# Kernel tuning notes

Hardware: AMD Instinct MI355X
Metric: run time of the kernel (lower is better)

The kernel has to match this reference:

```python
import jax, jax.numpy as jnp
import numpy as np

PATCH = 288
DIM = 2048
SCALE = DIM ** -0.5
NUM_INSTANCE = 4
B, Q, H, W = 32, 16, 24, 12


def _layernorm(x):
    # elementwise_affine=False LayerNorm, eps=1e-5
    m = jnp.mean(x, axis=-1, keepdims=True)
    v = jnp.mean((x - m) ** 2, axis=-1, keepdims=True)
    return (x - m) / jnp.sqrt(v + 1e-5)


def _l2norm(x):
    n = jnp.sqrt(jnp.sum(x * x, axis=-1, keepdims=True))
    return x / jnp.maximum(n, 1e-12)


def _catcher(x, g, cam_embed, Wq, Wg, pos_embed):
    # x: [B,Q,C] queries; g: [B,N,C] tokens; cam_embed: [B*N//PATCH,1,C] or None
    rel_q = jnp.einsum('bqc,dc->bqd', x, Wq)
    Bg, N, C = g.shape
    G = Bg * N // PATCH
    g2 = g.reshape(G, PATCH, C)
    rel = _l2norm(g2)
    rel = jax.nn.softmax(jnp.einsum('gpc,gqc->gpq', rel, rel), axis=-1)
    g2 = jnp.einsum('gpq,gqc->gpc', rel, g2)  # [G,PATCH,C]
    if cam_embed is not None:
        rel_g = g2 + cam_embed.reshape(G, 1, C)  # cam embed replaces pos embed (as in torch)
    else:
        rel_g = g2 + pos_embed
    g_out = g2.reshape(Bg, N, C)
    rel_g = jnp.einsum('bnc,dc->bnd', rel_g.reshape(Bg, N, C), Wg)
    att = jax.nn.softmax(jnp.einsum('bqc,bnc->bqn', rel_q, rel_g) * SCALE, axis=-1)
    out = jnp.einsum('bqn,bnc->bqc', att, g_out)
    return out, att


def _deltaor(x, g, Wq, Wg):
    q = _layernorm(x)
    rel_q = jnp.einsum('bqc,dc->bqd', q, Wq)
    g = g - jnp.mean(x, axis=1, keepdims=True)
    g = _layernorm(g)
    rel_g = jnp.einsum('bnc,dc->bnd', g, Wg)
    att = jax.nn.softmax(jnp.einsum('bqc,bnc->bqn', rel_q, rel_g) * SCALE, axis=-1)
    return x + jnp.einsum('bqn,bnc->bqc', att, g)


def setup_inputs() -> dict:
    key = jax.random.key(0)
    ks = jax.random.split(key, 12)
    w_scale = DIM ** -0.5
    return {
        'x': jax.random.normal(ks[0], (B, DIM, H, W), dtype=jnp.float32),
        'cam_ids': jax.random.randint(ks[1], (B,), 1, 7),
        'sub': jax.random.randint(ks[2], (B,), 0, 2).astype(bool),
        'query_v': 0.02 * jax.random.normal(ks[3], (1, Q, DIM), dtype=jnp.float32),
        'prototype': 0.02 * jax.random.normal(ks[4], (1, 2048, DIM), dtype=jnp.float32),
        'weights': jnp.ones((1, Q, 1), dtype=jnp.float32),
        'cam_table': 0.02 * jax.random.normal(ks[5], (6, 1, DIM), dtype=jnp.float32),
        'pos_embed': 0.02 * jax.random.normal(ks[6], (1, PATCH, DIM), dtype=jnp.float32),
        'Wcq': w_scale * jax.random.normal(ks[7], (DIM, DIM), dtype=jnp.float32),
        'Wcg': w_scale * jax.random.normal(ks[8], (DIM, DIM), dtype=jnp.float32),
        'Wdq': w_scale * jax.random.normal(ks[9], (DIM, DIM), dtype=jnp.float32),
        'Wdg': w_scale * jax.random.normal(ks[10], (DIM, DIM), dtype=jnp.float32),
    }


def reference(x, cam_ids, sub, query_v, prototype, weights, cam_table, pos_embed,
              Wcq, Wcg, Wdq, Wdg):
    Bx, C, Hx, Wx = x.shape
    HW = Hx * Wx
    xs = jnp.transpose(x.reshape(Bx, C, HW), (0, 2, 1))  # [B,HW,C]
    query = jnp.broadcast_to(query_v, (Bx,) + query_v.shape[1:])
    proto = jnp.broadcast_to(prototype, (Bx,) + prototype.shape[1:])
    cam_embed = cam_table[cam_ids - 1]  # [B,1,C]

    f_rel, _ = _catcher(query, xs, cam_embed, Wcq, Wcg, pos_embed)
    f_pro = _deltaor(f_rel, proto, Wdq, Wdg)

    # training branch (P2R shares weights with Q2R)
    f_rec, _ = _catcher(f_pro, xs, cam_embed, Wcq, Wcg, pos_embed)

    G = Bx // NUM_INSTANCE
    ce = cam_embed.reshape(G, 1, NUM_INSTANCE, 1, C)
    ce = jnp.broadcast_to(ce, (G, NUM_INSTANCE, NUM_INSTANCE, 1, C)).reshape(Bx, NUM_INSTANCE, C)
    xr = xs.reshape(G, 1, NUM_INSTANCE, HW, C)
    xr = jnp.broadcast_to(xr, (G, NUM_INSTANCE, NUM_INSTANCE, HW, C)).reshape(Bx, NUM_INSTANCE * HW, C)
    # torch.cat([a[~sub], a[sub]]) == stable sort by sub (False first)
    perm = jnp.argsort(sub.astype(jnp.int32))
    ce = ce[perm]
    xr = xr[perm]
    f_cor, _ = _catcher(f_pro, xr, ce, Wcq, Wcg, pos_embed)

    f_pro = jax.nn.softmax(weights, axis=1) * f_pro
    return f_rel, f_pro, f_rec, f_cor
```

## Files before the change

kernel.cpp:

```cpp
#include <hip/hip_runtime.h>
#include <math.h>

static constexpr float SCALE = 0.022097086912079612f;

typedef __bf16 bf16x2 __attribute__((ext_vector_type(2)));
typedef __bf16 bf16x4 __attribute__((ext_vector_type(4)));
typedef __bf16 bf16x8 __attribute__((ext_vector_type(8)));
typedef float  f32x2  __attribute__((ext_vector_type(2)));
typedef float  f32x4  __attribute__((ext_vector_type(4)));

__device__ __forceinline__ float wred_sum(float v){
  #pragma unroll
  for (int o=32;o>0;o>>=1) v += __shfl_down(v,o,64);
  return v;
}
__device__ __forceinline__ float wred_max(float v){
  #pragma unroll
  for (int o=32;o>0;o>>=1) v = fmaxf(v, __shfl_down(v,o,64));
  return v;
}
__device__ __forceinline__ float block_sum(float v, float* red){
  int tid=threadIdx.x, w=tid>>6, l=tid&63, nw=(int)(blockDim.x>>6);
  v = wred_sum(v);
  __syncthreads();
  if (l==0) red[w]=v;
  __syncthreads();
  float r=0.f;
  for (int i=0;i<nw;i++) r += red[i];
  return r;
}
__device__ __forceinline__ float block_max(float v, float* red){
  int tid=threadIdx.x, w=tid>>6, l=tid&63, nw=(int)(blockDim.x>>6);
  v = wred_max(v);
  __syncthreads();
  if (l==0) red[w]=v;
  __syncthreads();
  float r=red[0];
  for (int i=1;i<nw;i++) r = fmaxf(r, red[i]);
  return r;
}

template<int MT, int NT, int WM, int WN>
__global__ __launch_bounds__(256, 2)
void gemm_nt_mfma(float* __restrict__ Cm, const float* __restrict__ Am,
                  const float* __restrict__ Bm, int M, int N, int K,
                  int lda, int ldb, int ldc, long sA, long sB, long sC,
                  float alpha, const int* __restrict__ browidx, long sBrow,
                  int KS, float* __restrict__ Part,
                  __bf16* __restrict__ Chp, __bf16* __restrict__ Clp)
{
  constexpr int BM = MT*16*WM;
  constexpr int BN = NT*16*WN;
  constexpr int LDH = 40;
  constexpr int AST = (BM+31)/32;
  constexpr int BST = (BN+31)/32;
  __shared__ __bf16 Ah[BM*LDH];
  __shared__ __bf16 Al[BM*LDH];
  __shared__ __bf16 Bh[BN*LDH];
  __shared__ __bf16 Bl[BN*LDH];
  int ZZ = gridDim.z / KS;
  int z  = blockIdx.z % ZZ;
  int ks = blockIdx.z / ZZ;
  const float* A = Am + (long)z*sA;
  const float* B = Bm + (long)z*sB;
  float* C = Cm + (long)z*sC;
  const bool useB = (browidx != nullptr);
  const int* brow = useB ? (browidx + (long)z*sBrow) : nullptr;
  int Kc = ((K + KS*32 - 1) / (KS*32)) * 32;
  int kbeg = ks*Kc;
  int kend = min(K, kbeg + Kc);
  int m0 = blockIdx.y*BM, n0 = blockIdx.x*BN;
  int t = threadIdx.x;
  int srow = t>>3, skoff = (t&7)*4;

  float4 areg[AST], breg[BST];
  auto loadAB = [&](int k0){
    #pragma unroll
    for (int s=0;s<AST;++s){
      int row = srow + 32*s; int gm = m0+row;
      areg[s] = make_float4(0.f,0.f,0.f,0.f);
      if (row < BM && gm < M) areg[s] = *(const float4*)(A + (long)gm*lda + k0 + skoff);
    }
    #pragma unroll
    for (int s=0;s<BST;++s){
      int row = srow + 32*s; int gn = n0+row;
      breg[s] = make_float4(0.f,0.f,0.f,0.f);
      if (row < BN && gn < N){
        long r = useB ? (long)brow[gn] : (long)gn;
        breg[s] = *(const float4*)(B + r*ldb + k0 + skoff);
      }
    }
  };
  auto writeLDS = [&](){
    #pragma unroll
    for (int s=0;s<AST;++s){
      int row = srow + 32*s;
      if (row < BM){
        float vv[4] = {areg[s].x, areg[s].y, areg[s].z, areg[s].w};
        bf16x4 hv, lv;
        #pragma unroll
        for (int e=0;e<4;++e){
          __bf16 h = (__bf16)vv[e];
          hv[e] = h;
          lv[e] = (__bf16)(vv[e] - (float)h);
        }
        *(bf16x4*)&Ah[row*LDH + skoff] = hv;
        *(bf16x4*)&Al[row*LDH + skoff] = lv;
      }
    }
    #pragma unroll
    for (int s=0;s<BST;++s){
      int row = srow + 32*s;
      if (row < BN){
        float vv[4] = {breg[s].x, breg[s].y, breg[s].z, breg[s].w};
        bf16x4 hv, lv;
        #pragma unroll
        for (int e=0;e<4;++e){
          __bf16 h = (__bf16)vv[e];
          hv[e] = h;
          lv[e] = (__bf16)(vv[e] - (float)h);
        }
        *(bf16x4*)&Bh[row*LDH + skoff] = hv;
        *(bf16x4*)&Bl[row*LDH + skoff] = lv;
      }
    }
  };

  int lane = t & 63, wid = t >> 6;
  int wm = (WM==1) ? 0 : (wid / WN);
  int wn = wid % WN;
  int mw = wm*MT*16, nw = wn*NT*16;
  int fr = lane & 15, fq = (lane>>4)*8;

  f32x4 acc[MT][NT];
  #pragma unroll
  for (int i=0;i<MT;++i)
    #pragma unroll
    for (int j=0;j<NT;++j) acc[i][j] = (f32x4){0.f,0.f,0.f,0.f};

  if (kbeg < kend) loadAB(kbeg);
  for (int k0=kbeg; k0<kend; k0+=32){
    writeLDS();
    __syncthreads();
    if (k0+32 < kend) loadAB(k0+32);
    bf16x8 ah[MT], al[MT], bh[NT], bl[NT];
    #pragma unroll
    for (int i=0;i<MT;++i){
      ah[i] = *(const bf16x8*)&Ah[(mw+i*16+fr)*LDH + fq];
      al[i] = *(const bf16x8*)&Al[(mw+i*16+fr)*LDH + fq];
    }
    #pragma unroll
    for (int j=0;j<NT;++j){
      bh[j] = *(const bf16x8*)&Bh[(nw+j*16+fr)*LDH + fq];
      bl[j] = *(const bf16x8*)&Bl[(nw+j*16+fr)*LDH + fq];
    }
    #pragma unroll
    for (int i=0;i<MT;++i)
      #pragma unroll
      for (int j=0;j<NT;++j){
        acc[i][j] = __builtin_amdgcn_mfma_f32_16x16x32_bf16(ah[i], bh[j], acc[i][j], 0,0,0);
        acc[i][j] = __builtin_amdgcn_mfma_f32_16x16x32_bf16(ah[i], bl[j], acc[i][j], 0,0,0);
        acc[i][j] = __builtin_amdgcn_mfma_f32_16x16x32_bf16(al[i], bh[j], acc[i][j], 0,0,0);
      }
    __syncthreads();
  }
  float wf = (KS==1) ? alpha : 1.f;
  float* Cw = C; int ldw = ldc;
  if (ks > 0){ Cw = Part + ((long)(ks-1)*ZZ + z)*(long)M*N; ldw = N; }
  int er = (lane>>4)*4, ec = lane & 15;
  #pragma unroll
  for (int i=0;i<MT;++i){
    int mbase = m0 + mw + i*16 + er;
    #pragma unroll
    for (int r=0;r<4;++r){
      int mm = mbase + r;
      if (mm < M){
        long cro = (long)mm*ldw;
        #pragma unroll
        for (int j=0;j<NT;++j){
          int nn = n0 + nw + j*16 + ec;
          if (nn < N){
            float v = wf*acc[i][j][r];
            if (Chp){
              long po = (long)z*sC + cro + nn;
              __bf16 h = (__bf16)v;
              Chp[po] = h;
              Clp[po] = (__bf16)(v - (float)h);
            } else {
              Cw[cro + nn] = v;
            }
          }
        }
      }
    }
  }
}

template<int MT, int NT, int WM, int WN>
__global__ __launch_bounds__(256, 2)
void gemm_nt_bsg(float* __restrict__ Cm,
                 const __bf16* __restrict__ Ahg, const __bf16* __restrict__ Alg,
                 const __bf16* __restrict__ Bhg, const __bf16* __restrict__ Blg,
                 int M, int N, int K, int lda, int ldb, int ldc,
                 long sA, long sB, long sC,
                 float alpha, const int* __restrict__ browidx, long sBrow,
                 int KS, float* __restrict__ Part)
{
  constexpr int BM = MT*16*WM;
  constexpr int BN = NT*16*WN;
  constexpr int LDH = 40;
  __shared__ __bf16 Ah[BM*LDH];
  __shared__ __bf16 Al[BM*LDH];
  __shared__ __bf16 Bh[BN*LDH];
  __shared__ __bf16 Bl[BN*LDH];
  int ZZ = gridDim.z / KS;
  int z  = blockIdx.z % ZZ;
  int ks = blockIdx.z / ZZ;
  const __bf16* Ahb = Ahg + (long)z*sA;
  const __bf16* Alb = Alg + (long)z*sA;
  const __bf16* Bhb = Bhg + (long)z*sB;
  const __bf16* Blb = Blg + (long)z*sB;
  float* C = Cm + (long)z*sC;
  const bool useB = (browidx != nullptr);
  const int* brow = useB ? (browidx + (long)z*sBrow) : nullptr;
  int Kc = ((K + KS*32 - 1) / (KS*32)) * 32;
  int kbeg = ks*Kc;
  int kend = min(K, kbeg + Kc);
  int m0 = blockIdx.y*BM, n0 = blockIdx.x*BN;
  int t = threadIdx.x;
  constexpr int ASl = (BM*4 + 255)/256;
  constexpr int BSl = (BN*4 + 255)/256;
  bf16x8 arh[ASl], arl[ASl], brh[BSl], brl[BSl];
  bf16x8 zed;
  #pragma unroll
  for (int e=0;e<8;++e) zed[e] = (__bf16)0.f;

  auto loadAB = [&](int k0){
    #pragma unroll
    for (int i=0;i<ASl;++i){
      int s = t + 256*i;
      arh[i] = zed; arl[i] = zed;
      if (s < BM*4){
        int row = s>>2, koff = (s&3)*8; int gm = m0+row;
        if (gm < M){
          long off = (long)gm*lda + k0 + koff;
          arh[i] = *(const bf16x8*)(Ahb + off);
          arl[i] = *(const bf16x8*)(Alb + off);
        }
      }
    }
    #pragma unroll
    for (int i=0;i<BSl;++i){
      int s = t + 256*i;
      brh[i] = zed; brl[i] = zed;
      if (s < BN*4){
        int row = s>>2, koff = (s&3)*8; int gn = n0+row;
        if (gn < N){
          long r = useB ? (long)brow[gn] : (long)gn;
          long off = r*ldb + k0 + koff;
          brh[i] = *(const bf16x8*)(Bhb + off);
          brl[i] = *(const bf16x8*)(Blb + off);
        }
      }
    }
  };
  auto writeLDS = [&](){
    #pragma unroll
    for (int i=0;i<ASl;++i){
      int s = t + 256*i;
      if (s < BM*4){
        int row = s>>2, koff = (s&3)*8;
        *(bf16x8*)&Ah[row*LDH + koff] = arh[i];
        *(bf16x8*)&Al[row*LDH + koff] = arl[i];
      }
    }
    #pragma unroll
    for (int i=0;i<BSl;++i){
      int s = t + 256*i;
      if (s < BN*4){
        int row = s>>2, koff = (s&3)*8;
        *(bf16x8*)&Bh[row*LDH + koff] = brh[i];
        *(bf16x8*)&Bl[row*LDH + koff] = brl[i];
      }
    }
  };

  int lane = t & 63, wid = t >> 6;
  int wm = (WM==1) ? 0 : (wid / WN);
  int wn = wid % WN;
  int mw = wm*MT*16, nw = wn*NT*16;
  int fr = lane & 15, fq = (lane>>4)*8;

  f32x4 acc[MT][NT];
  #pragma unroll
  for (int i=0;i<MT;++i)
    #pragma unroll
    for (int j=0;j<NT;++j) acc[i][j] = (f32x4){0.f,0.f,0.f,0.f};

  if (kbeg < kend) loadAB(kbeg);
  for (int k0=kbeg; k0<kend; k0+=32){
    writeLDS();
    __syncthreads();
    if (k0+32 < kend) loadAB(k0+32);
    bf16x8 ah[MT], al[MT], bh[NT], bl[NT];
    #pragma unroll
    for (int i=0;i<MT;++i){
      ah[i] = *(const bf16x8*)&Ah[(mw+i*16+fr)*LDH + fq];
      al[i] = *(const bf16x8*)&Al[(mw+i*16+fr)*LDH + fq];
    }
    #pragma unroll
    for (int j=0;j<NT;++j){
      bh[j] = *(const bf16x8*)&Bh[(nw+j*16+fr)*LDH + fq];
      bl[j] = *(const bf16x8*)&Bl[(nw+j*16+fr)*LDH + fq];
    }
    #pragma unroll
    for (int i=0;i<MT;++i)
      #pragma unroll
      for (int j=0;j<NT;++j){
        acc[i][j] = __builtin_amdgcn_mfma_f32_16x16x32_bf16(ah[i], bh[j], acc[i][j], 0,0,0);
        acc[i][j] = __builtin_amdgcn_mfma_f32_16x16x32_bf16(ah[i], bl[j], acc[i][j], 0,0,0);
        acc[i][j] = __builtin_amdgcn_mfma_f32_16x16x32_bf16(al[i], bh[j], acc[i][j], 0,0,0);
      }
    __syncthreads();
  }
  float wf = (KS==1) ? alpha : 1.f;
  float* Cw = C; int ldw = ldc;
  if (ks > 0){ Cw = Part + ((long)(ks-1)*ZZ + z)*(long)M*N; ldw = N; }
  int er = (lane>>4)*4, ec = lane & 15;
  #pragma unroll
  for (int i=0;i<MT;++i){
    int mbase = m0 + mw + i*16 + er;
    #pragma unroll
    for (int r=0;r<4;++r){
      int mm = mbase + r;
      if (mm < M){
        long cro = (long)mm*ldw;
        #pragma unroll
        for (int j=0;j<NT;++j){
          int nn = n0 + nw + j*16 + ec;
          if (nn < N) Cw[cro + nn] = wf*acc[i][j][r];
        }
      }
    }
  }
}

__global__ __launch_bounds__(256) void k_reduce(float* __restrict__ C, const float* __restrict__ Part,
                                                long total, int S, float alpha){
  for (long i = (long)blockIdx.x*blockDim.x + threadIdx.x; i < total;
       i += (long)gridDim.x*blockDim.x){
    float v = C[i];
    for (int s=0;s<S;++s) v += Part[(long)s*total + i];
    C[i] = alpha*v;
  }
}

__global__ __launch_bounds__(256) void k_reduce_split(float* __restrict__ C, const float* __restrict__ Part,
                                                      long total, int S, float alpha,
                                                      __bf16* __restrict__ H, __bf16* __restrict__ L){
  long n4 = total >> 2;
  for (long i = (long)blockIdx.x*blockDim.x + threadIdx.x; i < n4;
       i += (long)gridDim.x*blockDim.x){
    float4 v = ((float4*)C)[i];
    for (int s=0;s<S;++s){
      float4 p = ((const float4*)(Part + (long)s*total))[i];
      v.x += p.x; v.y += p.y; v.z += p.z; v.w += p.w;
    }
    v.x *= alpha; v.y *= alpha; v.z *= alpha; v.w *= alpha;
    ((float4*)C)[i] = v;
    float vv[4] = {v.x, v.y, v.z, v.w};
    bf16x4 h, l;
    #pragma unroll
    for (int e=0;e<4;++e){
      __bf16 hh = (__bf16)vv[e];
      h[e] = hh;
      l[e] = (__bf16)(vv[e] - (float)hh);
    }
    ((bf16x4*)H)[i] = h;
    ((bf16x4*)L)[i] = l;
  }
}

__global__ __launch_bounds__(256) void k_split(const float* __restrict__ X,
                                               __bf16* __restrict__ H, __bf16* __restrict__ L, long n){
  long n4 = n >> 2;
  for (long i = (long)blockIdx.x*blockDim.x + threadIdx.x; i < n4;
       i += (long)gridDim.x*blockDim.x){
    float4 v = ((const float4*)X)[i];
    float vv[4] = {v.x, v.y, v.z, v.w};
    bf16x4 h, l;
    #pragma unroll
    for (int e=0;e<4;++e){
      __bf16 hh = (__bf16)vv[e];
      h[e] = hh;
      l[e] = (__bf16)(vv[e] - (float)hh);
    }
    ((bf16x4*)H)[i] = h;
    ((bf16x4*)L)[i] = l;
  }
}

__global__ __launch_bounds__(256, 2) void k_pv2(
    float* __restrict__ C, float* __restrict__ Part,
    const float* __restrict__ Pm, long sP, int K, int Kc,
    const __bf16* __restrict__ Gh, const __bf16* __restrict__ Gl,
    long sG, const int* __restrict__ SB)
{
  extern __shared__ float Pl[];
  int b = blockIdx.y, ks = blockIdx.z;
  int kbeg = ks * Kc;
  int kend = min(K, kbeg + Kc);
  int len = kend - kbeg;
  int c0 = blockIdx.x*512 + threadIdx.x*2;
  const float* Pb = Pm + (long)b*sP;
  for (int i = threadIdx.x; i < 16*len; i += 256){
    int q = i / len, kk = i - q*len;
    Pl[q*Kc + kk] = Pb[(long)q*K + kbeg + kk];
  }
  __syncthreads();
  f32x2 acc[16];
  #pragma unroll
  for (int q=0;q<16;++q) acc[q] = (f32x2){0.f,0.f};
  int kk = 0;
  while (kk < len){
    int kg = kbeg + kk;
    int seg = kg / 288;
    int row = kg - seg*288;
    int nrow = min(288 - row, len - kk);
    long base = (SB ? (long)SB[(b<<2)+seg]*sG : (long)b*sG) + (long)row*2048 + c0;
    const __bf16* gh = Gh + base;
    const __bf16* gl = Gl + base;
    bf16x2 h0,h1,h2,h3,l0,l1,l2,l3;
    h0 = *(const bf16x2*)(gh);       l0 = *(const bf16x2*)(gl);
    h1 = *(const bf16x2*)(gh+2048);  l1 = *(const bf16x2*)(gl+2048);
    h2 = *(const bf16x2*)(gh+4096);  l2 = *(const bf16x2*)(gl+4096);
    h3 = *(const bf16x2*)(gh+6144);  l3 = *(const bf16x2*)(gl+6144);
    gh += 8192; gl += 8192;
    for (int r = 0; r < nrow; r += 4, kk += 4){
      bf16x2 nh0=h0,nh1=h1,nh2=h2,nh3=h3,nl0=l0,nl1=l1,nl2=l2,nl3=l3;
      if (r + 4 < nrow){
        nh0 = *(const bf16x2*)(gh);       nl0 = *(const bf16x2*)(gl);
        nh1 = *(const bf16x2*)(gh+2048);  nl1 = *(const bf16x2*)(gl+2048);
        nh2 = *(const bf16x2*)(gh+4096);  nl2 = *(const bf16x2*)(gl+4096);
        nh3 = *(const bf16x2*)(gh+6144);  nl3 = *(const bf16x2*)(gl+6144);
        gh += 8192; gl += 8192;
      }
      f32x2 g0, g1, g2, g3;
      g0[0]=(float)h0[0]+(float)l0[0]; g0[1]=(float)h0[1]+(float)l0[1];
      g1[0]=(float)h1[0]+(float)l1[0]; g1[1]=(float)h1[1]+(float)l1[1];
      g2[0]=(float)h2[0]+(float)l2[0]; g2[1]=(float)h2[1]+(float)l2[1];
      g3[0]=(float)h3[0]+(float)l3[0]; g3[1]=(float)h3[1]+(float)l3[1];
      #pragma unroll
      for (int q=0;q<16;++q){
        f32x4 p = *(const f32x4*)&Pl[q*Kc + kk];
        acc[q] += p[0]*g0;
        acc[q] += p[1]*g1;
        acc[q] += p[2]*g2;
        acc[q] += p[3]*g3;
      }
      h0=nh0; h1=nh1; h2=nh2; h3=nh3;
      l0=nl0; l1=nl1; l2=nl2; l3=nl3;
    }
  }
  float* Cw = (ks==0) ? C : (Part + (long)(ks-1)*1048576);
  long obase = (long)b*32768 + c0;
  #pragma unroll
  for (int q=0;q<16;++q) *(f32x2*)&Cw[obase + (long)q*2048] = acc[q];
}

__global__ void k_tr(const float* __restrict__ in, float* __restrict__ out, int R, int C){
  __shared__ float tile[32][33];
  long zo = (long)blockIdx.z * R * C;
  int r0 = blockIdx.y*32, c0 = blockIdx.x*32;
  int tx = threadIdx.x, ty = threadIdx.y;
  #pragma unroll
  for (int j=0;j<32;j+=8)
    tile[ty+j][tx] = in[zo + (long)(r0+ty+j)*C + c0+tx];
  __syncthreads();
  #pragma unroll
  for (int j=0;j<32;j+=8)
    out[zo + (long)(c0+ty+j)*R + r0+tx] = tile[tx][ty+j];
}

__global__ void k_tr_split(const float* __restrict__ in, __bf16* __restrict__ oh,
                           __bf16* __restrict__ ol, int R, int C){
  __shared__ float tile[32][33];
  int r0 = blockIdx.y*32, c0 = blockIdx.x*32;
  int tx = threadIdx.x, ty = threadIdx.y;
  #pragma unroll
  for (int j=0;j<32;j+=8)
    tile[ty+j][tx] = in[(long)(r0+ty+j)*C + c0+tx];
  __syncthreads();
  #pragma unroll
  for (int j=0;j<32;j+=8){
    float v = tile[tx][ty+j];
    __bf16 h = (__bf16)v;
    long idx = (long)(c0+ty+j)*R + r0+tx;
    oh[idx] = h;
    ol[idx] = (__bf16)(v - (float)h);
  }
}

__global__ __launch_bounds__(256) void k_rowstats(const float* __restrict__ X, long ldx, int cols,
                                                  float* __restrict__ mu, float* __restrict__ m2){
  int r = blockIdx.x;
  const float* row = X + (long)r*ldx;
  float s=0.f, s2=0.f;
  for (int c = threadIdx.x*4; c < cols; c += 1024){
    float4 v = *(const float4*)(row+c);
    s  += v.x+v.y+v.z+v.w;
    s2 += v.x*v.x+v.y*v.y+v.z*v.z+v.w*v.w;
  }
  __shared__ float red[8];
  s  = block_sum(s,  red);
  s2 = block_sum(s2, red);
  if (threadIdx.x==0){ mu[r]=s/(float)cols; m2[r]=s2; }
}

__global__ __launch_bounds__(256) void k_softmax_gram(float* __restrict__ S, const float* __restrict__ Part,
                                                      const float* __restrict__ m2xs){
  int r = blockIdx.x;
  int b = r / 288, p = r % 288;
  float* row = S + (long)r * 288;
  const float* prow = Part + (long)b*82944 + (long)p*288;
  const float* m2 = m2xs + (long)b*288;
  float rp = 1.f / fmaxf(sqrtf(m2[p]), 1e-12f);
  int tid = threadIdx.x;
  __shared__ float red[8];
  float lv[2];
  #pragma unroll
  for (int i=0;i<2;++i){
    int q = tid + i*256;
    lv[i] = (q<288) ? (row[q]+prow[q])*rp/fmaxf(sqrtf(m2[q]),1e-12f) : -1e30f;
  }
  float mx = fmaxf(lv[0], lv[1]);
  mx = block_max(mx, red);
  float s = 0.f;
  #pragma unroll
  for (int i=0;i<2;++i){
    int q = tid + i*256;
    float e = (q<288) ? expf(lv[i]-mx) : 0.f;
    lv[i]=e; s+=e;
  }
  s = block_sum(s, red);
  float inv = 1.f/s;
  #pragma unroll
  for (int i=0;i<2;++i){ int q = tid + i*256; if (q<288) row[q]=lv[i]*inv; }
}

__global__ __launch_bounds__(256) void k_softmax_plain_r(float* __restrict__ X,
                                                         const float* __restrict__ Part,
                                                         int S, float alpha){
  int r = blockIdx.x; int b = r>>4, qq = r&15;
  float* row = X + (long)r * 288;
  int tid = threadIdx.x;
  __shared__ float red[8];
  float lv[2];
  #pragma unroll
  for (int i=0;i<2;++i){
    int q = tid + i*256;
    if (q<288){
      float v = row[q];
      for (int s=0;s<S;++s) v += Part[((long)s*32 + b)*4608 + (long)qq*288 + q];
      lv[i] = v*alpha;
    } else lv[i] = -1e30f;
  }
  float mx = fmaxf(lv[0], lv[1]);
  mx = block_max(mx, red);
  float s = 0.f;
  #pragma unroll
  for (int i=0;i<2;++i){ int q = tid + i*256; float e = (q<288)?expf(lv[i]-mx):0.f; lv[i]=e; s+=e; }
  s = block_sum(s, red);
  float inv = 1.f/s;
  #pragma unroll
  for (int i=0;i<2;++i){ int q = tid + i*256; if (q<288) row[q]=lv[i]*inv; }
}

__global__ __launch_bounds__(256) void k_softmax_seg(float* __restrict__ X, const float* __restrict__ PartS,
                                                     int Ss,
                                                     const float* __restrict__ CC,
                                                     const float* __restrict__ PartC, int Sc,
                                                     const int* __restrict__ SB, float scale){
  int r = blockIdx.x; int b = r>>4, qq = r&15;
  float* row = X + (long)r*1152;
  float bias[4];
  #pragma unroll
  for (int j=0;j<4;++j){
    int col = SB[b*4+j];
    float cv = CC[(long)r*32 + col];
    for (int s=0;s<Sc;++s) cv += PartC[(long)s*16384 + (long)r*32 + col];
    bias[j] = scale*cv;
  }
  int tid = threadIdx.x;
  __shared__ float red[8];
  float lv[5];
  #pragma unroll
  for (int i=0;i<5;++i){
    int q = tid + i*256;
    if (q<1152){
      float v = row[q];
      for (int s=0;s<Ss;++s) v += PartS[((long)s*32 + b)*18432 + (long)qq*1152 + q];
      lv[i] = v*scale + bias[q/288];
    } else lv[i] = -1e30f;
  }
  float mx = -1e30f;
  #pragma unroll
  for (int i=0;i<5;++i) mx = fmaxf(mx, lv[i]);
  mx = block_max(mx, red);
  float s = 0.f;
  #pragma unroll
  for (int i=0;i<5;++i){ int q = tid + i*256; float e = (q<1152)?expf(lv[i]-mx):0.f; lv[i]=e; s+=e; }
  s = block_sum(s, red);
  float inv = 1.f/s;
  #pragma unroll
  for (int i=0;i<5;++i){ int q = tid + i*256; if (q<1152) row[q]=lv[i]*inv; }
}

__global__ void k_ln_apply_s(const float* __restrict__ X, const float* __restrict__ mu,
                             const float* __restrict__ m2, __bf16* __restrict__ H,
                             __bf16* __restrict__ L){
  int r = blockIdx.y; int c = blockIdx.x*256 + threadIdx.x;
  float m = mu[r];
  float v = m2[r]*(1.f/2048.f) - m*m;
  float inv = rsqrtf(v + 1e-5f);
  long idx = (long)r*2048 + c;
  float y = (X[idx] - m)*inv;
  __bf16 h = (__bf16)y;
  H[idx] = h;
  L[idx] = (__bf16)(y - (float)h);
}

__global__ void k_meanx(const float* __restrict__ frel, float* __restrict__ mx){
  int b = blockIdx.y; int c = blockIdx.x*256 + threadIdx.x;
  const float* base = frel + (long)b*16*2048 + c;
  float s=0.f;
  #pragma unroll
  for (int q=0;q<16;++q) s += base[(long)q*2048];
  mx[(long)b*2048 + c] = s * (1.f/16.f);
}

__global__ void k_sigma(const float* __restrict__ pm, const float* __restrict__ mu_p,
                        const float* __restrict__ m2_p, const float* __restrict__ mu_m,
                        const float* __restrict__ m2_m, float* __restrict__ sigma){
  int b = blockIdx.y; int n = blockIdx.x*256 + threadIdx.x;
  float mp = mu_p[n], mm = mu_m[b];
  float vp = m2_p[n]*(1.f/2048.f) - mp*mp;
  float vm = m2_m[b]*(1.f/2048.f) - mm*mm;
  float cov = pm[(long)b*2048+n]*(1.f/2048.f) - mp*mm;
  sigma[(long)b*2048+n] = sqrtf(fmaxf(vp + vm - 2.f*cov, 0.f) + 1e-5f);
}

__global__ void k_fixrow(float* __restrict__ X, const float* __restrict__ mu_row,
                         const float* __restrict__ mu_w){
  int r = blockIdx.y; int d = blockIdx.x*256 + threadIdx.x;
  X[(long)r*2048 + d] -= mu_row[r] * mu_w[d] * 2048.f;
}

__global__ __launch_bounds__(256) void k_qm2(const float* __restrict__ relq2,
                                             const float* __restrict__ Mx,
                                             const float* __restrict__ muw,
                                             float* __restrict__ qm, float* __restrict__ qw){
  int r = blockIdx.x; int b = r >> 4;
  const float* a = relq2 + (long)r*2048;
  const float* m = Mx + (long)b*2048;
  float s=0.f, sw=0.f;
  for (int c = threadIdx.x*4; c < 2048; c += 1024){
    float4 va=*(const float4*)(a+c), vm=*(const float4*)(m+c), vw=*(const float4*)(muw+c);
    s  += va.x*vm.x+va.y*vm.y+va.z*vm.z+va.w*vm.w;
    sw += va.x*vw.x+va.y*vw.y+va.z*vw.z+va.w*vw.w;
  }
  __shared__ float red[8];
  s  = block_sum(s,  red);
  sw = block_sum(sw, red);
  if (threadIdx.x==0){ qm[r]=s; qw[r]=sw; }
}

__global__ __launch_bounds__(256) void k_score2_s(const float* __restrict__ QPw, const float* __restrict__ qm,
                                                  const float* __restrict__ qw,
                                                  const float* __restrict__ sigma, const float* __restrict__ mu_p,
                                                  __bf16* __restrict__ QH, __bf16* __restrict__ QL,
                                                  float* __restrict__ W1, float* __restrict__ Wmu, float scale){
  int r = blockIdx.x; int b = r >> 4;
  const float* row = QPw + (long)r*2048;
  const float* sg = sigma + (long)b*2048;
  int tid = threadIdx.x;
  __shared__ float red[8];
  float qmr = qm[r];
  float qwr2048 = 2048.f * qw[r];
  float lv[8], ls[8], lmp[8];
  #pragma unroll
  for (int i=0;i<8;++i){
    int n = tid + i*256;
    float sgn = sg[n];
    float mpn = mu_p[n];
    ls[i] = sgn;
    lmp[i] = mpn;
    lv[i] = scale * (row[n] - qwr2048*mpn - qmr) / sgn;
  }
  float mx = -1e30f;
  #pragma unroll
  for (int i=0;i<8;++i) mx = fmaxf(mx, lv[i]);
  mx = block_max(mx, red);
  float se=0.f, sw=0.f, swm=0.f;
  #pragma unroll
  for (int i=0;i<8;++i){
    float e = expf(lv[i]-mx);
    lv[i] = e; se += e;
    float wv = e/ls[i];
    sw += wv; swm += wv*lmp[i];
  }
  se  = block_sum(se,  red);
  sw  = block_sum(sw,  red);
  swm = block_sum(swm, red);
  float inv = 1.f/se;
  #pragma unroll
  for (int i=0;i<8;++i){
    int n = tid + i*256;
    float v = lv[i]*inv/ls[i];
    __bf16 h = (__bf16)v;
    long idx = (long)r*2048 + n;
    QH[idx] = h;
    QL[idx] = (__bf16)(v - (float)h);
  }
  if (tid==0){ W1[r]=sw*inv; Wmu[r]=swm*inv; }
}

__global__ void k_fpro_final_s(const float* __restrict__ frel, const float* __restrict__ out2,
                               const float* __restrict__ meanx, const float* __restrict__ mu_m,
                               const float* __restrict__ W1, const float* __restrict__ Wmu,
                               const float* __restrict__ wsm,
                               __bf16* __restrict__ FH, __bf16* __restrict__ FL,
                               float* __restrict__ fout){
  int r = blockIdx.y; int c = blockIdx.x*256 + threadIdx.x;
  int b = r >> 4, q = r & 15;
  long idx = (long)r*2048 + c;
  float w1 = W1[r];
  float v = frel[idx] + out2[idx] - meanx[(long)b*2048+c]*w1 - Wmu[r] + mu_m[b]*w1;
  __bf16 h = (__bf16)v;
  FH[idx] = h;
  FL[idx] = (__bf16)(v - (float)h);
  fout[idx] = wsm[q] * v;
}

__global__ void k_camb(const float* __restrict__ cam_table, const int* __restrict__ cam_ids,
                       __bf16* __restrict__ H, __bf16* __restrict__ L){
  int b = blockIdx.y; int c = blockIdx.x*256 + threadIdx.x;
  float v = cam_table[(long)(cam_ids[b]-1)*2048 + c];
  __bf16 h = (__bf16)v;
  long idx = (long)b*2048 + c;
  H[idx] = h;
  L[idx] = (__bf16)(v - (float)h);
}

__global__ void k_wsoft(const float* __restrict__ w, float* __restrict__ wsm){
  if (threadIdx.x==0){
    float mx=-1e30f;
    for (int i=0;i<16;++i) mx=fmaxf(mx,w[i]);
    float e[16], s=0.f;
    for (int i=0;i<16;++i){ e[i]=expf(w[i]-mx); s+=e[i]; }
    for (int i=0;i<16;++i) wsm[i]=e[i]/s;
  }
}

__global__ void k_perm(const void* __restrict__ subp, int* __restrict__ gidx, int* __restrict__ SB){
  __shared__ int perm[32];
  if (threadIdx.x==0){
    const int* pi = (const int*)subp;
    const float* pf = (const float*)subp;
    const unsigned char* pb = (const unsigned char*)subp;
    int sv[32]; bool okI=true, okF=true;
    for (int i=0;i<32;++i){ int v=pi[i]; if (v!=0 && v!=1) okI=false; }
    for (int i=0;i<32;++i){ float f=pf[i]; if (f!=0.f && f!=1.f) okF=false; }
    for (int i=0;i<32;++i){
      if (okI) sv[i]=pi[i];
      else if (okF) sv[i]=(pf[i]!=0.f)?1:0;
      else sv[i]=(pb[i]!=0)?1:0;
    }
    int pos=0;
    for (int i=0;i<32;++i) if (!sv[i]) perm[pos++]=i;
    for (int i=0;i<32;++i) if ( sv[i]) perm[pos++]=i;
  }
  __syncthreads();
  for (int i = threadIdx.x; i < 128; i += blockDim.x){
    int b = i>>2, j = i&3;
    SB[i] = ((perm[b]>>2)<<2) + j;
  }
  for (int idx = threadIdx.x; idx < 32*1152; idx += blockDim.x){
    int b = idx / 1152, rem = idx % 1152, j = rem / 288, n = rem % 288;
    int src = ((perm[b] >> 2) << 2) + j;
    gidx[idx] = src*288 + n;
  }
}

extern "C" void kernel_launch(void* const* d_in, const int* in_sizes, int n_in,
                              void* d_out, int out_size, void* d_ws, size_t ws_size,
                              hipStream_t stream) {
  const float* x        = (const float*)d_in[0];
  const int*   cam_ids  = (const int*)d_in[1];
  const void*  subp     = d_in[2];
  const float* query_v  = (const float*)d_in[3];
  const float* proto    = (const float*)d_in[4];
  const float* weights  = (const float*)d_in[5];
  const float* cam_tab  = (const float*)d_in[6];
  const float* Wcq      = (const float*)d_in[8];
  const float* Wcg      = (const float*)d_in[9];
  const float* Wdq      = (const float*)d_in[10];
  const float* Wdg      = (const float*)d_in[11];
  float* out = (float*)d_out;
  float* ws  = (float*)d_ws;

  size_t o = 0;
  float* S     = ws + o; o += 2654208;
  __bf16* QLNh   = (__bf16*)S;
  __bf16* QLNl   = (__bf16*)(S + 524288);
  __bf16* RELQ2h = (__bf16*)(S + 1048576);
  __bf16* RELQ2l = (__bf16*)(S + 1572864);
  float* XSR   = ws + o; o += 18874368;
  float* XS    = XSR;
  float* PART  = XSR;
  __bf16* WCQh  = (__bf16*)(XSR + 6291456);
  __bf16* WCQl  = (__bf16*)(XSR + 8388608);
  __bf16* WCGTh = (__bf16*)(XSR + 10485760);
  __bf16* WCGTl = (__bf16*)(XSR + 12582912);
  __bf16* ROTh  = (__bf16*)(XSR + 14680064);
  __bf16* ROTl  = (__bf16*)(XSR + 16777216);
  float* GMIXR = ws + o; o += 18874368;
  __bf16* GMIXh = (__bf16*)GMIXR;
  __bf16* GMIXl = GMIXh + 18874368;
  float* MU_XS = ws + o; o += 9216;
  float* M2_XS = ws + o; o += 9216;
  float* CAMB  = ws + o; o += 65536;
  __bf16* CAMBh = (__bf16*)CAMB;
  __bf16* CAMBl = CAMBh + 65536;
  float* RQ0   = ws + o; o += 32768;
  float* RQW   = ws + o; o += 32768;
  float* SREL  = ws + o; o += 147456;
  float* MU_FR = ws + o; o += 512;
  float* M2_FR = ws + o; o += 512;
  float* T1    = ws + o; o += 1048576;
  float* RELQ2 = ws + o; o += 1048576;
  float* MEANX = ws + o; o += 65536;
  float* MU_P  = ws + o; o += 2048;
  float* M2_P  = ws + o; o += 2048;
  float* MU_M  = ws + o; o += 64;
  float* M2_M  = ws + o; o += 64;
  float* MU_W  = ws + o; o += 2048;
  float* M2_W  = ws + o; o += 2048;
  float* PM    = ws + o; o += 65536;
  float* SIGMA = ws + o; o += 65536;
  float* MX    = ws + o; o += 65536;
  float* QP    = ws + o; o += 1048576;
  float* QM    = ws + o; o += 512;
  float* QW    = ws + o; o += 512;
  float* W1    = ws + o; o += 512;
  float* WMU   = ws + o; o += 512;
  float* OUT2  = ws + o; o += 1048576;
  __bf16* FPROh = (__bf16*)(ws + o);
  __bf16* FPROl = (__bf16*)(ws + o + 524288); o += 1048576;
  float* RQ2   = ws + o; o += 1048576;
  float* RQW2  = ws + o; o += 1048576;
  __bf16* RQW2h = (__bf16*)(ws + o);
  __bf16* RQW2l = RQW2h + 1048576; o += 1048576;
  float* SREC  = ws + o; o += 147456;
  float* SCOR  = ws + o; o += 589824;
  float* CC    = ws + o; o += 16384;
  float* WSM   = ws + o; o += 16;
  __bf16* T1h   = (__bf16*)(ws + o);
  __bf16* T1l   = (__bf16*)(ws + o + 524288); o += 1048576;
  __bf16* QPWh  = (__bf16*)(ws + o);
  __bf16* QPWl  = (__bf16*)(ws + o + 524288); o += 1048576;
  __bf16* RQ2h  = (__bf16*)(ws + o);
  __bf16* RQ2l  = (__bf16*)(ws + o + 524288); o += 1048576;
  __bf16* QVh   = (__bf16*)(ws + o);
  __bf16* QVl   = (__bf16*)(ws + o + 16384); o += 32768;
  __bf16* RQ0h  = (__bf16*)(ws + o);
  __bf16* RQ0l  = (__bf16*)(ws + o + 16384); o += 32768;
  __bf16* RQWh  = (__bf16*)(ws + o);
  __bf16* RQWl  = RQWh + 32768; o += 32768;
  int*   GIDX  = (int*)(ws + o); o += 36864;
  int*   SB    = (int*)(ws + o); o += 128;

  float* F_REL = out;
  float* F_PRO = out + 1048576;
  float* F_REC = out + 2097152;
  float* F_COR = out + 3145728;

  float* PART_CC = PART + 4000000;

  k_tr<<<dim3(9,64,32), dim3(32,8), 0, stream>>>(x, XS, 2048, 288);
  k_rowstats<<<9216, 256, 0, stream>>>(XS, 2048, 2048, MU_XS, M2_XS);
  gemm_nt_mfma<3,3,2,2><<<dim3(3,3,64), 256, 0, stream>>>(S, XS, XS, 288,288,2048,
      2048,2048,288, 589824,589824,82944, 1.f, nullptr,0, 2, GMIXR, nullptr, nullptr);
  k_softmax_gram<<<9216, 256, 0, stream>>>(S, GMIXR, M2_XS);
  gemm_nt_mfma<3,4,2,2><<<dim3(16,3,32), 256, 0, stream>>>(GMIXR, S, x, 288,2048,288,
      288,288,2048, 82944,589824,589824, 1.f, nullptr,0, 1, nullptr, GMIXh, GMIXl);
  k_split<<<2048, 256, 0, stream>>>(Wcq, WCQh, WCQl, 4194304L);
  k_tr_split<<<dim3(64,64), dim3(32,8), 0, stream>>>(Wcg, WCGTh, WCGTl, 2048, 2048);
  k_split<<<32, 256, 0, stream>>>(query_v, QVh, QVl, 32768L);
  k_camb<<<dim3(8,32), 256, 0, stream>>>(cam_tab, cam_ids, CAMBh, CAMBl);
  k_perm<<<1, 256, 0, stream>>>(subp, GIDX, SB);
  k_wsoft<<<1, 64, 0, stream>>>(weights, WSM);

  gemm_nt_bsg<1,4,1,4><<<dim3(8,1,16), 256, 0, stream>>>(RQ0, QVh,QVl, WCQh,WCQl,
      16,2048,2048, 2048,2048,2048, 0,0,0, 1.f, nullptr,0, 16, PART);
  k_reduce_split<<<64, 256, 0, stream>>>(RQ0, PART, 32768L, 15, 1.f, RQ0h, RQ0l);
  gemm_nt_bsg<1,4,1,4><<<dim3(8,1,16), 256, 0, stream>>>(RQW, RQ0h,RQ0l, WCGTh,WCGTl,
      16,2048,2048, 2048,2048,2048, 0,0,0, 1.f, nullptr,0, 16, PART);
  k_reduce_split<<<64, 256, 0, stream>>>(RQW, PART, 32768L, 15, 1.f, RQWh, RQWl);
  gemm_nt_bsg<1,4,1,4><<<dim3(2,1,256), 256, 0, stream>>>(SREL, RQWh,RQWl, GMIXh,GMIXl,
      16,288,2048, 2048,2048,288, 0,589824,4608, SCALE, nullptr,0, 8, PART);
  k_softmax_plain_r<<<512, 256, 0, stream>>>(SREL, PART, 7, SCALE);
  k_pv2<<<dim3(4,32,7), 256, 16*44*4, stream>>>(F_REL, PART, SREL, 4608, 288, 44,
      GMIXh, GMIXl, 589824, nullptr);
  k_reduce<<<1024, 256, 0, stream>>>(F_REL, PART, 1048576L, 6, 1.f);

  k_rowstats<<<512, 256, 0, stream>>>(F_REL, 2048, 2048, MU_FR, M2_FR);
  k_ln_apply_s<<<dim3(8,512), 256, 0, stream>>>(F_REL, MU_FR, M2_FR, QLNh, QLNl);
  k_meanx<<<dim3(8,32), 256, 0, stream>>>(F_REL, MEANX);
  k_rowstats<<<32,   256, 0, stream>>>(MEANX, 2048, 2048, MU_M, M2_M);
  k_rowstats<<<2048, 256, 0, stream>>>(proto, 2048, 2048, MU_P, M2_P);
  k_rowstats<<<2048, 256, 0, stream>>>(Wdg,   2048, 2048, MU_W, M2_W);
  k_split<<<2048, 256, 0, stream>>>(Wdq, ROTh, ROTl, 4194304L);
  gemm_nt_bsg<2,2,2,2><<<dim3(32,8,3), 256, 0, stream>>>(RELQ2, QLNh,QLNl, ROTh,ROTl,
      512,2048,2048, 2048,2048,2048, 0,0,0, 1.f, nullptr,0, 3, PART);
  k_reduce_split<<<1024, 256, 0, stream>>>(RELQ2, PART, 1048576L, 2, 1.f, RELQ2h, RELQ2l);
  gemm_nt_mfma<1,4,1,4><<<dim3(8,2,8), 256, 0, stream>>>(PM, MEANX, proto, 32,2048,2048,
      2048,2048,2048, 0,0,0, 1.f, nullptr,0, 8, PART, nullptr, nullptr);
  k_reduce<<<256, 256, 0, stream>>>(PM, PART, 65536L, 7, 1.f);
  k_sigma<<<dim3(8,32), 256, 0, stream>>>(PM, MU_P, M2_P, MU_M, M2_M, SIGMA);
  k_tr_split<<<dim3(64,64), dim3(32,8), 0, stream>>>(Wdg, ROTh, ROTl, 2048, 2048);
  gemm_nt_bsg<2,2,2,2><<<dim3(32,8,3), 256, 0, stream>>>(T1, RELQ2h,RELQ2l, ROTh,ROTl,
      512,2048,2048, 2048,2048,2048, 0,0,0, 1.f, nullptr,0, 3, PART);
  k_reduce_split<<<1024, 256, 0, stream>>>(T1, PART, 1048576L, 2, 1.f, T1h, T1l);
  gemm_nt_mfma<1,4,1,4><<<dim3(8,2,8), 256, 0, stream>>>(MX, MEANX, Wdg, 32,2048,2048,
      2048,2048,2048, 0,0,0, 1.f, nullptr,0, 8, PART, nullptr, nullptr);
  k_reduce<<<256, 256, 0, stream>>>(MX, PART, 65536L, 7, 1.f);
  k_fixrow<<<dim3(8,32), 256, 0, stream>>>(MX, MU_M, MU_W);
  k_split<<<2048, 256, 0, stream>>>(proto, ROTh, ROTl, 4194304L);
  gemm_nt_bsg<2,2,2,2><<<dim3(32,8,3), 256, 0, stream>>>(QP, T1h,T1l, ROTh,ROTl,
      512,2048,2048, 2048,2048,2048, 0,0,0, 1.f, nullptr,0, 3, PART);
  k_reduce<<<1024, 256, 0, stream>>>(QP, PART, 1048576L, 2, 1.f);
  k_qm2<<<512, 256, 0, stream>>>(RELQ2, MX, MU_W, QM, QW);
  k_score2_s<<<512, 256, 0, stream>>>(QP, QM, QW, SIGMA, MU_P, QPWh, QPWl, W1, WMU, SCALE);
  k_tr_split<<<dim3(64,64), dim3(32,8), 0, stream>>>(proto, ROTh, ROTl, 2048, 2048);
  gemm_nt_bsg<2,2,2,2><<<dim3(32,8,3), 256, 0, stream>>>(OUT2, QPWh,QPWl, ROTh,ROTl,
      512,2048,2048, 2048,2048,2048, 0,0,0, 1.f, nullptr,0, 3, PART);
  k_reduce<<<1024, 256, 0, stream>>>(OUT2, PART, 1048576L, 2, 1.f);
  k_fpro_final_s<<<dim3(8,512), 256, 0, stream>>>(F_REL, OUT2, MEANX, MU_M, W1, WMU, WSM,
                                                  FPROh, FPROl, F_PRO);

  gemm_nt_bsg<2,2,2,2><<<dim3(32,8,3), 256, 0, stream>>>(RQ2, FPROh,FPROl, WCQh,WCQl,
      512,2048,2048, 2048,2048,2048, 0,0,0, 1.f, nullptr,0, 3, PART);
  k_reduce_split<<<1024, 256, 0, stream>>>(RQ2, PART, 1048576L, 2, 1.f, RQ2h, RQ2l);
  gemm_nt_bsg<2,2,2,2><<<dim3(32,8,3), 256, 0, stream>>>(RQW2, RQ2h,RQ2l, WCGTh,WCGTl,
      512,2048,2048, 2048,2048,2048, 0,0,0, 1.f, nullptr,0, 3, PART);
  k_reduce_split<<<1024, 256, 0, stream>>>(RQW2, PART, 1048576L, 2, 1.f, RQW2h, RQW2l);
  gemm_nt_bsg<1,4,1,4><<<dim3(2,1,256), 256, 0, stream>>>(SREC, RQW2h,RQW2l, GMIXh,GMIXl,
      16,288,2048, 2048,2048,288, 32768,589824,4608, SCALE, nullptr,0, 8, PART);
  k_softmax_plain_r<<<512, 256, 0, stream>>>(SREC, PART, 7, SCALE);
  k_pv2<<<dim3(4,32,7), 256, 16*44*4, stream>>>(F_REC, PART, SREC, 4608, 288, 44,
      GMIXh, GMIXl, 589824, nullptr);
  k_reduce<<<1024, 256, 0, stream>>>(F_REC, PART, 1048576L, 6, 1.f);

  gemm_nt_bsg<1,4,1,4><<<dim3(1,32,8), 256, 0, stream>>>(CC, RQW2h,RQW2l, CAMBh,CAMBl,
      512,32,2048, 2048,2048,32, 0,0,0, 1.f, nullptr,0, 8, PART_CC);
  gemm_nt_bsg<1,4,1,4><<<dim3(5,1,128), 256, 0, stream>>>(SCOR, RQW2h,RQW2l, GMIXh,GMIXl,
      16,1152,2048, 2048,2048,1152, 32768,0,18432, SCALE, GIDX,1152, 4, PART);
  k_softmax_seg<<<512, 256, 0, stream>>>(SCOR, PART, 3, CC, PART_CC, 7, SB, SCALE);
  k_pv2<<<dim3(4,32,7), 256, 16*168*4, stream>>>(F_COR, PART, SCOR, 18432, 1152, 168,
      GMIXh, GMIXl, 589824, SB);
  k_reduce<<<1024, 256, 0, stream>>>(F_COR, PART, 1048576L, 6, 1.f);
}
```

Measured before the change: 984.9 us.

## Fuse small kernels, pre-split Gram inputs to bf16 pairs, vectorize reductions

The transpose now writes bf16 hi/lo splits and accumulates squared norms atomically, so the Gram GEMM reads pre-split bf16 instead of fp32. A dedicated gmix GEMM consumes the bf16-split softmax output. Row-stats, layernorm, mean, sigma, qm and score kernels are merged, with split-K partial reductions folded into their consumers. Scalar reductions become float4. The aim is fewer launches and less HBM traffic, at the cost of atomics and more complex kernels.

Result: faster. 918.6 us (-6.7%).

```diff
diff --git a/kernel.cpp b/kernel.cpp
--- a/kernel.cpp
+++ b/kernel.cpp
@@ -45,9 +45,7 @@
 void gemm_nt_mfma(float* __restrict__ Cm, const float* __restrict__ Am,
                   const float* __restrict__ Bm, int M, int N, int K,
                   int lda, int ldb, int ldc, long sA, long sB, long sC,
-                  float alpha, const int* __restrict__ browidx, long sBrow,
-                  int KS, float* __restrict__ Part,
-                  __bf16* __restrict__ Chp, __bf16* __restrict__ Clp)
+                  float alpha, int KS, float* __restrict__ Part)
 {
   constexpr int BM = MT*16*WM;
   constexpr int BN = NT*16*WN;
@@ -64,8 +62,6 @@
   const float* A = Am + (long)z*sA;
   const float* B = Bm + (long)z*sB;
   float* C = Cm + (long)z*sC;
-  const bool useB = (browidx != nullptr);
-  const int* brow = useB ? (browidx + (long)z*sBrow) : nullptr;
   int Kc = ((K + KS*32 - 1) / (KS*32)) * 32;
   int kbeg = ks*Kc;
   int kend = min(K, kbeg + Kc);
@@ -85,10 +81,7 @@
     for (int s=0;s<BST;++s){
       int row = srow + 32*s; int gn = n0+row;
       breg[s] = make_float4(0.f,0.f,0.f,0.f);
-      if (row < BN && gn < N){
-        long r = useB ? (long)brow[gn] : (long)gn;
-        breg[s] = *(const float4*)(B + r*ldb + k0 + skoff);
-      }
+      if (row < BN && gn < N) breg[s] = *(const float4*)(B + (long)gn*ldb + k0 + skoff);
     }
   };
   auto writeLDS = [&](){
@@ -179,17 +172,7 @@
         #pragma unroll
         for (int j=0;j<NT;++j){
           int nn = n0 + nw + j*16 + ec;
-          if (nn < N){
-            float v = wf*acc[i][j][r];
-            if (Chp){
-              long po = (long)z*sC + cro + nn;
-              __bf16 h = (__bf16)v;
-              Chp[po] = h;
-              Clp[po] = (__bf16)(v - (float)h);
-            } else {
-              Cw[cro + nn] = v;
-            }
-          }
+          if (nn < N) Cw[cro + nn] = wf*acc[i][j][r];
         }
       }
     }
@@ -345,13 +328,135 @@
   }
 }
 
-__global__ __launch_bounds__(256) void k_reduce(float* __restrict__ C, const float* __restrict__ Part,
-                                                long total, int S, float alpha){
-  for (long i = (long)blockIdx.x*blockDim.x + threadIdx.x; i < total;
+__global__ __launch_bounds__(256, 2)
+void gemm_gmix(const __bf16* __restrict__ Sh, const __bf16* __restrict__ Sl,
+               const float* __restrict__ xg,
+               __bf16* __restrict__ Gh, __bf16* __restrict__ Gl)
+{
+  constexpr int BM = 96, BN = 128, LDH = 40;
+  __shared__ __bf16 Ah[BM*LDH];
+  __shared__ __bf16 Al[BM*LDH];
+  __shared__ __bf16 Bh[BN*LDH];
+  __shared__ __bf16 Bl[BN*LDH];
+  int z = blockIdx.z;
+  const __bf16* Azh = Sh + (long)z*82944;
+  const __bf16* Azl = Sl + (long)z*82944;
+  const float*  B   = xg + (long)z*589824;
+  int m0 = blockIdx.y*BM, n0 = blockIdx.x*BN;
+  int t = threadIdx.x;
+  int srow = t>>3, skoff = (t&7)*4;
+  bf16x8 arh[2], arl[2];
+  float4 breg[4];
+  auto loadAB = [&](int k0){
+    #pragma unroll
+    for (int i=0;i<2;++i){
+      int s = t + 256*i;
+      if (s < 384){
+        int row = s>>2, koff = (s&3)*8;
+        long off = (long)(m0+row)*288 + k0 + koff;
+        arh[i] = *(const bf16x8*)(Azh + off);
+        arl[i] = *(const bf16x8*)(Azl + off);
+      }
+    }
+    #pragma unroll
+    for (int si=0;si<4;++si){
+      int row = srow + 32*si;
+      breg[si] = *(const float4*)(B + (long)(n0+row)*288 + k0 + skoff);
+    }
+  };
+  auto writeLDS = [&](){
+    #pragma unroll
+    for (int i=0;i<2;++i){
+      int s = t + 256*i;
+      if (s < 384){
+        int row = s>>2, koff = (s&3)*8;
+        *(bf16x8*)&Ah[row*LDH + koff] = arh[i];
+        *(bf16x8*)&Al[row*LDH + koff] = arl[i];
+      }
+    }
+    #pragma unroll
+    for (int si=0;si<4;++si){
+      int row = srow + 32*si;
+      float vv[4] = {breg[si].x, breg[si].y, breg[si].z, breg[si].w};
+      bf16x4 hv, lv;
+      #pragma unroll
+      for (int e=0;e<4;++e){
+        __bf16 h = (__bf16)vv[e];
+        hv[e] = h;
+        lv[e] = (__bf16)(vv[e] - (float)h);
+      }
+      *(bf16x4*)&Bh[row*LDH + skoff] = hv;
+      *(bf16x4*)&Bl[row*LDH + skoff] = lv;
+    }
+  };
+  int lane = t & 63, wid = t >> 6;
+  int wm = wid >> 1, wn = wid & 1;
+  int mw = wm*48, nw = wn*64;
+  int fr = lane & 15, fq = (lane>>4)*8;
+  f32x4 acc[3][4];
+  #pragma unroll
+  for (int i=0;i<3;++i)
+    #pragma unroll
+    for (int j=0;j<4;++j) acc[i][j] = (f32x4){0.f,0.f,0.f,0.f};
+
+  loadAB(0);
+  for (int k0=0; k0<288; k0+=32){
+    writeLDS();
+    __syncthreads();
+    if (k0+32 < 288) loadAB(k0+32);
+    bf16x8 ah[3], al[3], bh[4], bl[4];
+    #pragma unroll
+    for (int i=0;i<3;++i){
+      ah[i] = *(const bf16x8*)&Ah[(mw+i*16+fr)*LDH + fq];
+      al[i] = *(const bf16x8*)&Al[(mw+i*16+fr)*LDH + fq];
+    }
+    #pragma unroll
+    for (int j=0;j<4;++j){
+      bh[j] = *(const bf16x8*)&Bh[(nw+j*16+fr)*LDH + fq];
+      bl[j] = *(const bf16x8*)&Bl[(nw+j*16+fr)*LDH + fq];
+    }
+    #pragma unroll
+    for (int i=0;i<3;++i)
+      #pragma unroll
+      for (int j=0;j<4;++j){
+        acc[i][j] = __builtin_amdgcn_mfma_f32_16x16x32_bf16(ah[i], bh[j], acc[i][j], 0,0,0);
+        acc[i][j] = __builtin_amdgcn_mfma_f32_16x16x32_bf16(ah[i], bl[j], acc[i][j], 0,0,0);
+        acc[i][j] = __builtin_amdgcn_mfma_f32_16x16x32_bf16(al[i], bh[j], acc[i][j], 0,0,0);
+      }
+    __syncthreads();
+  }
+  int er = (lane>>4)*4, ec = lane & 15;
+  #pragma unroll
+  for (int i=0;i<3;++i){
+    int mbase = m0 + mw + i*16 + er;
+    #pragma unroll
+    for (int r=0;r<4;++r){
+      int mm = mbase + r;
+      long ro = (long)z*589824 + (long)mm*2048;
+      #pragma unroll
+      for (int j=0;j<4;++j){
+        int nn = n0 + nw + j*16 + ec;
+        float v = acc[i][j][r];
+        __bf16 h = (__bf16)v;
+        Gh[ro + nn] = h;
+        Gl[ro + nn] = (__bf16)(v - (float)h);
+      }
+    }
+  }
+}
+
+__global__ __launch_bounds__(256) void k_reduce4(float* __restrict__ C, const float* __restrict__ Part,
+                                                 long total, int S, float alpha){
+  long n4 = total >> 2;
+  for (long i = (long)blockIdx.x*blockDim.x + threadIdx.x; i < n4;
        i += (long)gridDim.x*blockDim.x){
-    float v = C[i];
-    for (int s=0;s<S;++s) v += Part[(long)s*total + i];
-    C[i] = alpha*v;
+    float4 v = ((float4*)C)[i];
+    for (int s=0;s<S;++s){
+      float4 p = ((const float4*)(Part + (long)s*total))[i];
+      v.x += p.x; v.y += p.y; v.z += p.z; v.w += p.w;
+    }
+    v.x *= alpha; v.y *= alpha; v.z *= alpha; v.w *= alpha;
+    ((float4*)C)[i] = v;
   }
 }
 
@@ -468,18 +573,37 @@
   for (int q=0;q<16;++q) *(f32x2*)&Cw[obase + (long)q*2048] = acc[q];
 }
 
-__global__ void k_tr(const float* __restrict__ in, float* __restrict__ out, int R, int C){
+__global__ void k_trs(const float* __restrict__ in, __bf16* __restrict__ oh,
+                      __bf16* __restrict__ ol, float* __restrict__ m2){
   __shared__ float tile[32][33];
-  long zo = (long)blockIdx.z * R * C;
+  __shared__ float cred[8][33];
+  int bz = blockIdx.z;
+  long zo = (long)bz*589824;
   int r0 = blockIdx.y*32, c0 = blockIdx.x*32;
   int tx = threadIdx.x, ty = threadIdx.y;
-  #pragma unroll
-  for (int j=0;j<32;j+=8)
-    tile[ty+j][tx] = in[zo + (long)(r0+ty+j)*C + c0+tx];
+  float ss = 0.f;
+  #pragma unroll
+  for (int j=0;j<32;j+=8){
+    float v = in[zo + (long)(r0+ty+j)*288 + c0+tx];
+    tile[ty+j][tx] = v;
+    ss += v*v;
+  }
+  cred[ty][tx] = ss;
   __syncthreads();
   #pragma unroll
-  for (int j=0;j<32;j+=8)
-    out[zo + (long)(c0+ty+j)*R + r0+tx] = tile[tx][ty+j];
+  for (int j=0;j<32;j+=8){
+    float v = tile[tx][ty+j];
+    __bf16 h = (__bf16)v;
+    long idx = zo + (long)(c0+ty+j)*2048 + r0+tx;
+    oh[idx] = h;
+    ol[idx] = (__bf16)(v - (float)h);
+  }
+  if (ty==0){
+    float s = cred[0][tx];
+    #pragma unroll
+    for (int k=1;k<8;++k) s += cred[k][tx];
+    atomicAdd(&m2[bz*288 + c0+tx], s);
+  }
 }
 
 __global__ void k_tr_split(const float* __restrict__ in, __bf16* __restrict__ oh,
@@ -501,12 +625,15 @@
   }
 }
 
-__global__ __launch_bounds__(256) void k_rowstats(const float* __restrict__ X, long ldx, int cols,
-                                                  float* __restrict__ mu, float* __restrict__ m2){
+__global__ __launch_bounds__(256) void k_rowstats2(const float* __restrict__ X1, const float* __restrict__ X2,
+                                                   float* __restrict__ mu1, float* __restrict__ m21,
+                                                   float* __restrict__ mu2, float* __restrict__ m22){
   int r = blockIdx.x;
-  const float* row = X + (long)r*ldx;
+  const float* row; float* mu; float* m2; int idx;
+  if (r < 2048){ idx = r; row = X1 + (long)idx*2048; mu = mu1; m2 = m21; }
+  else { idx = r - 2048; row = X2 + (long)idx*2048; mu = mu2; m2 = m22; }
   float s=0.f, s2=0.f;
-  for (int c = threadIdx.x*4; c < cols; c += 1024){
+  for (int c = threadIdx.x*4; c < 2048; c += 1024){
     float4 v = *(const float4*)(row+c);
     s  += v.x+v.y+v.z+v.w;
     s2 += v.x*v.x+v.y*v.y+v.z*v.z+v.w*v.w;
@@ -514,14 +641,15 @@
   __shared__ float red[8];
   s  = block_sum(s,  red);
   s2 = block_sum(s2, red);
-  if (threadIdx.x==0){ mu[r]=s/(float)cols; m2[r]=s2; }
-}
-
-__global__ __launch_bounds__(256) void k_softmax_gram(float* __restrict__ S, const float* __restrict__ Part,
-                                                      const float* __restrict__ m2xs){
+  if (threadIdx.x==0){ mu[idx]=s*(1.f/2048.f); m2[idx]=s2; }
+}
+
+__global__ __launch_bounds__(256) void k_softmax_gram_s(const float* __restrict__ S, const float* __restrict__ Part,
+                                                        const float* __restrict__ m2xs,
+                                                        __bf16* __restrict__ Hh, __bf16* __restrict__ Hl){
   int r = blockIdx.x;
   int b = r / 288, p = r % 288;
-  float* row = S + (long)r * 288;
+  const float* row = S + (long)r * 288;
   const float* prow = Part + (long)b*82944 + (long)p*288;
   const float* m2 = m2xs + (long)b*288;
   float rp = 1.f / fmaxf(sqrtf(m2[p]), 1e-12f);
@@ -545,7 +673,16 @@
   s = block_sum(s, red);
   float inv = 1.f/s;
   #pragma unroll
-  for (int i=0;i<2;++i){ int q = tid + i*256; if (q<288) row[q]=lv[i]*inv; }
+  for (int i=0;i<2;++i){
+    int q = tid + i*256;
+    if (q<288){
+      float v = lv[i]*inv;
+      __bf16 h = (__bf16)v;
+      long idx = (long)r*288 + q;
+      Hh[idx] = h;
+      Hl[idx] = (__bf16)(v - (float)h);
+    }
+  }
 }
 
 __global__ __launch_bounds__(256) void k_softmax_plain_r(float* __restrict__ X,
@@ -616,86 +753,127 @@
   for (int i=0;i<5;++i){ int q = tid + i*256; if (q<1152) row[q]=lv[i]*inv; }
 }
 
-__global__ void k_ln_apply_s(const float* __restrict__ X, const float* __restrict__ mu,
-                             const float* __restrict__ m2, __bf16* __restrict__ H,
-                             __bf16* __restrict__ L){
-  int r = blockIdx.y; int c = blockIdx.x*256 + threadIdx.x;
-  float m = mu[r];
-  float v = m2[r]*(1.f/2048.f) - m*m;
-  float inv = rsqrtf(v + 1e-5f);
-  long idx = (long)r*2048 + c;
-  float y = (X[idx] - m)*inv;
-  __bf16 h = (__bf16)y;
-  H[idx] = h;
-  L[idx] = (__bf16)(y - (float)h);
-}
-
-__global__ void k_meanx(const float* __restrict__ frel, float* __restrict__ mx){
-  int b = blockIdx.y; int c = blockIdx.x*256 + threadIdx.x;
-  const float* base = frel + (long)b*16*2048 + c;
-  float s=0.f;
-  #pragma unroll
-  for (int q=0;q<16;++q) s += base[(long)q*2048];
-  mx[(long)b*2048 + c] = s * (1.f/16.f);
-}
-
-__global__ void k_sigma(const float* __restrict__ pm, const float* __restrict__ mu_p,
-                        const float* __restrict__ m2_p, const float* __restrict__ mu_m,
-                        const float* __restrict__ m2_m, float* __restrict__ sigma){
+__global__ __launch_bounds__(256) void k_finalize_frel(float* __restrict__ F, const float* __restrict__ Part,
+                                                       int S, __bf16* __restrict__ H, __bf16* __restrict__ L){
+  int r = blockIdx.x;
+  long ro = (long)r*2048;
+  int tid = threadIdx.x;
+  float4 vbuf[2];
+  float s=0.f, s2=0.f;
+  #pragma unroll
+  for (int i=0;i<2;++i){
+    long c = (long)tid*4 + i*1024;
+    float4 a = *(const float4*)&F[ro+c];
+    for (int ss=0; ss<S; ++ss){
+      float4 p = *(const float4*)&Part[(long)ss*1048576 + ro + c];
+      a.x += p.x; a.y += p.y; a.z += p.z; a.w += p.w;
+    }
+    vbuf[i] = a;
+    *(float4*)&F[ro+c] = a;
+    s  += a.x+a.y+a.z+a.w;
+    s2 += a.x*a.x+a.y*a.y+a.z*a.z+a.w*a.w;
+  }
+  __shared__ float red[8];
+  s  = block_sum(s,  red);
+  s2 = block_sum(s2, red);
+  float m = s*(1.f/2048.f);
+  float var = s2*(1.f/2048.f) - m*m;
+  float inv = rsqrtf(var + 1e-5f);
+  #pragma unroll
+  for (int i=0;i<2;++i){
+    long c = (long)tid*4 + i*1024;
+    float vv[4] = {vbuf[i].x, vbuf[i].y, vbuf[i].z, vbuf[i].w};
+    bf16x4 h, l;
+    #pragma unroll
+    for (int e=0;e<4;++e){
+      float y = (vv[e]-m)*inv;
+      __bf16 hh = (__bf16)y;
+      h[e] = hh;
+      l[e] = (__bf16)(y - (float)hh);
+    }
+    *(bf16x4*)&H[ro+c] = h;
+    *(bf16x4*)&L[ro+c] = l;
+  }
+}
+
+__global__ __launch_bounds__(256) void k_meanx_stats(const float* __restrict__ frel, float* __restrict__ mx,
+                                                     float* __restrict__ mu_m, float* __restrict__ m2_m){
+  int b = blockIdx.x;
+  const float* base = frel + (long)b*32768;
+  int tid = threadIdx.x;
+  float s=0.f, s2=0.f;
+  #pragma unroll
+  for (int i=0;i<2;++i){
+    long c = (long)tid*4 + i*1024;
+    float4 a = make_float4(0.f,0.f,0.f,0.f);
+    #pragma unroll
+    for (int q=0;q<16;++q){
+      float4 v = *(const float4*)&base[(long)q*2048 + c];
+      a.x += v.x; a.y += v.y; a.z += v.z; a.w += v.w;
+    }
+    a.x *= (1.f/16.f); a.y *= (1.f/16.f); a.z *= (1.f/16.f); a.w *= (1.f/16.f);
+    *(float4*)&mx[(long)b*2048 + c] = a;
+    s  += a.x+a.y+a.z+a.w;
+    s2 += a.x*a.x+a.y*a.y+a.z*a.z+a.w*a.w;
+  }
+  __shared__ float red[8];
+  s  = block_sum(s,  red);
+  s2 = block_sum(s2, red);
+  if (tid==0){ mu_m[b]=s*(1.f/2048.f); m2_m[b]=s2; }
+}
+
+__global__ void k_sigma_r(const float* __restrict__ pm, const float* __restrict__ PartPM, int Sp,
+                          const float* __restrict__ mu_p, const float* __restrict__ m2_p,
+                          const float* __restrict__ mu_m, const float* __restrict__ m2_m,
+                          float* __restrict__ sigma){
   int b = blockIdx.y; int n = blockIdx.x*256 + threadIdx.x;
+  float pmv = pm[(long)b*2048+n];
+  for (int s=0;s<Sp;++s) pmv += PartPM[(long)s*65536 + (long)b*2048 + n];
   float mp = mu_p[n], mm = mu_m[b];
   float vp = m2_p[n]*(1.f/2048.f) - mp*mp;
   float vm = m2_m[b]*(1.f/2048.f) - mm*mm;
-  float cov = pm[(long)b*2048+n]*(1.f/2048.f) - mp*mm;
+  float cov = pmv*(1.f/2048.f) - mp*mm;
   sigma[(long)b*2048+n] = sqrtf(fmaxf(vp + vm - 2.f*cov, 0.f) + 1e-5f);
 }
 
-__global__ void k_fixrow(float* __restrict__ X, const float* __restrict__ mu_row,
-                         const float* __restrict__ mu_w){
-  int r = blockIdx.y; int d = blockIdx.x*256 + threadIdx.x;
-  X[(long)r*2048 + d] -= mu_row[r] * mu_w[d] * 2048.f;
-}
-
-__global__ __launch_bounds__(256) void k_qm2(const float* __restrict__ relq2,
-                                             const float* __restrict__ Mx,
-                                             const float* __restrict__ muw,
-                                             float* __restrict__ qm, float* __restrict__ qw){
+__global__ __launch_bounds__(256) void k_score2f(const float* __restrict__ QP, const float* __restrict__ QPpart, int Sq,
+                                                 const float* __restrict__ relq2,
+                                                 const float* __restrict__ MX, const float* __restrict__ MXpart, int Sm,
+                                                 const float* __restrict__ muw, const float* __restrict__ mu_m,
+                                                 const float* __restrict__ sigma, const float* __restrict__ mu_p,
+                                                 __bf16* __restrict__ QH, __bf16* __restrict__ QL,
+                                                 float* __restrict__ W1, float* __restrict__ Wmu, float scale){
   int r = blockIdx.x; int b = r >> 4;
-  const float* a = relq2 + (long)r*2048;
-  const float* m = Mx + (long)b*2048;
-  float s=0.f, sw=0.f;
-  for (int c = threadIdx.x*4; c < 2048; c += 1024){
-    float4 va=*(const float4*)(a+c), vm=*(const float4*)(m+c), vw=*(const float4*)(muw+c);
-    s  += va.x*vm.x+va.y*vm.y+va.z*vm.z+va.w*vm.w;
-    sw += va.x*vw.x+va.y*vw.y+va.z*vw.z+va.w*vw.w;
-  }
-  __shared__ float red[8];
-  s  = block_sum(s,  red);
-  sw = block_sum(sw, red);
-  if (threadIdx.x==0){ qm[r]=s; qw[r]=sw; }
-}
-
-__global__ __launch_bounds__(256) void k_score2_s(const float* __restrict__ QPw, const float* __restrict__ qm,
-                                                  const float* __restrict__ qw,
-                                                  const float* __restrict__ sigma, const float* __restrict__ mu_p,
-                                                  __bf16* __restrict__ QH, __bf16* __restrict__ QL,
-                                                  float* __restrict__ W1, float* __restrict__ Wmu, float scale){
-  int r = blockIdx.x; int b = r >> 4;
-  const float* row = QPw + (long)r*2048;
-  const float* sg = sigma + (long)b*2048;
   int tid = threadIdx.x;
   __shared__ float red[8];
-  float qmr = qm[r];
-  float qwr2048 = 2048.f * qw[r];
+  float qm=0.f, qw=0.f;
+  for (int c = tid*4; c < 2048; c += 1024){
+    float4 va = *(const float4*)&relq2[(long)r*2048 + c];
+    float4 vm = *(const float4*)&MX[(long)b*2048 + c];
+    for (int s=0;s<Sm;++s){
+      float4 p = *(const float4*)&MXpart[(long)s*65536 + (long)b*2048 + c];
+      vm.x += p.x; vm.y += p.y; vm.z += p.z; vm.w += p.w;
+    }
+    float4 vw = *(const float4*)&muw[c];
+    qm += va.x*vm.x+va.y*vm.y+va.z*vm.z+va.w*vm.w;
+    qw += va.x*vw.x+va.y*vw.y+va.z*vw.z+va.w*vw.w;
+  }
+  qm = block_sum(qm, red);
+  qw = block_sum(qw, red);
+  float qmr = qm - 2048.f*mu_m[b]*qw;
+  float qwr2048 = 2048.f*qw;
+  const float* sg = sigma + (long)b*2048;
   float lv[8], ls[8], lmp[8];
   #pragma unroll
   for (int i=0;i<8;++i){
     int n = tid + i*256;
+    float qpv = QP[(long)r*2048 + n];
+    for (int s=0;s<Sq;++s) qpv += QPpart[(long)s*1048576 + (long)r*2048 + n];
     float sgn = sg[n];
     float mpn = mu_p[n];
     ls[i] = sgn;
     lmp[i] = mpn;
-    lv[i] = scale * (row[n] - qwr2048*mpn - qmr) / sgn;
+    lv[i] = scale * (qpv - qwr2048*mpn - qmr) / sgn;
   }
   float mx = -1e30f;
   #pragma unroll
@@ -752,17 +930,8 @@
   L[idx] = (__bf16)(v - (float)h);
 }
 
-__global__ void k_wsoft(const float* __restrict__ w, float* __restrict__ wsm){
-  if (threadIdx.x==0){
-    float mx=-1e30f;
-    for (int i=0;i<16;++i) mx=fmaxf(mx,w[i]);
-    float e[16], s=0.f;
-    for (int i=0;i<16;++i){ e[i]=expf(w[i]-mx); s+=e[i]; }
-    for (int i=0;i<16;++i) wsm[i]=e[i]/s;
-  }
-}
-
-__global__ void k_perm(const void* __restrict__ subp, int* __restrict__ gidx, int* __restrict__ SB){
+__global__ void k_permw(const void* __restrict__ subp, const float* __restrict__ w,
+                        int* __restrict__ gidx, int* __restrict__ SB, float* __restrict__ wsm){
   __shared__ int perm[32];
   if (threadIdx.x==0){
     const int* pi = (const int*)subp;
@@ -779,6 +948,11 @@
     int pos=0;
     for (int i=0;i<32;++i) if (!sv[i]) perm[pos++]=i;
     for (int i=0;i<32;++i) if ( sv[i]) perm[pos++]=i;
+    float mx=-1e30f;
+    for (int i=0;i<16;++i) mx=fmaxf(mx,w[i]);
+    float e[16], s=0.f;
+    for (int i=0;i<16;++i){ e[i]=expf(w[i]-mx); s+=e[i]; }
+    for (int i=0;i<16;++i) wsm[i]=e[i]/s;
   }
   __syncthreads();
   for (int i = threadIdx.x; i < 128; i += blockDim.x){
@@ -816,7 +990,10 @@
   __bf16* RELQ2h = (__bf16*)(S + 1048576);
   __bf16* RELQ2l = (__bf16*)(S + 1572864);
   float* XSR   = ws + o; o += 18874368;
-  float* XS    = XSR;
+  __bf16* XSh = (__bf16*)XSR;
+  __bf16* XSl = XSh + 18874368;
+  __bf16* Shp = (__bf16*)XSR;
+  __bf16* Slp = Shp + 2654208;
   float* PART  = XSR;
   __bf16* WCQh  = (__bf16*)(XSR + 6291456);
   __bf16* WCQl  = (__bf16*)(XSR + 8388608);
@@ -827,7 +1004,6 @@
   float* GMIXR = ws + o; o += 18874368;
   __bf16* GMIXh = (__bf16*)GMIXR;
   __bf16* GMIXl = GMIXh + 18874368;
-  float* MU_XS = ws + o; o += 9216;
   float* M2_XS = ws + o; o += 9216;
   float* CAMB  = ws + o; o += 65536;
   __bf16* CAMBh = (__bf16*)CAMB;
@@ -835,8 +1011,6 @@
   float* RQ0   = ws + o; o += 32768;
   float* RQW   = ws + o; o += 32768;
   float* SREL  = ws + o; o += 147456;
-  float* MU_FR = ws + o; o += 512;
-  float* M2_FR = ws + o; o += 512;
   float* T1    = ws + o; o += 1048576;
   float* RELQ2 = ws + o; o += 1048576;
   float* MEANX = ws + o; o += 65536;
@@ -850,8 +1024,6 @@
   float* SIGMA = ws + o; o += 65536;
   float* MX    = ws + o; o += 65536;
   float* QP    = ws + o; o += 1048576;
-  float* QM    = ws + o; o += 512;
-  float* QW    = ws + o; o += 512;
   float* W1    = ws + o; o += 512;
   float* WMU   = ws + o; o += 512;
   float* OUT2  = ws + o; o += 1048576;
@@ -886,20 +1058,19 @@
   float* F_COR = out + 3145728;
 
   float* PART_CC = PART + 4000000;
-
-  k_tr<<<dim3(9,64,32), dim3(32,8), 0, stream>>>(x, XS, 2048, 288);
-  k_rowstats<<<9216, 256, 0, stream>>>(XS, 2048, 2048, MU_XS, M2_XS);
-  gemm_nt_mfma<3,3,2,2><<<dim3(3,3,64), 256, 0, stream>>>(S, XS, XS, 288,288,2048,
-      2048,2048,288, 589824,589824,82944, 1.f, nullptr,0, 2, GMIXR, nullptr, nullptr);
-  k_softmax_gram<<<9216, 256, 0, stream>>>(S, GMIXR, M2_XS);
-  gemm_nt_mfma<3,4,2,2><<<dim3(16,3,32), 256, 0, stream>>>(GMIXR, S, x, 288,2048,288,
-      288,288,2048, 82944,589824,589824, 1.f, nullptr,0, 1, nullptr, GMIXh, GMIXl);
+  float* PART_MX = PART + 3145728;
+
+  hipMemsetAsync(M2_XS, 0, 9216*sizeof(float), stream);
+  k_trs<<<dim3(9,64,32), dim3(32,8), 0, stream>>>(x, XSh, XSl, M2_XS);
+  gemm_nt_bsg<3,3,2,2><<<dim3(3,3,64), 256, 0, stream>>>(S, XSh,XSl, XSh,XSl,
+      288,288,2048, 2048,2048,288, 589824,589824,82944, 1.f, nullptr,0, 2, GMIXR);
+  k_softmax_gram_s<<<9216, 256, 0, stream>>>(S, GMIXR, M2_XS, Shp, Slp);
+  gemm_gmix<<<dim3(16,3,32), 256, 0, stream>>>(Shp, Slp, x, GMIXh, GMIXl);
   k_split<<<2048, 256, 0, stream>>>(Wcq, WCQh, WCQl, 4194304L);
   k_tr_split<<<dim3(64,64), dim3(32,8), 0, stream>>>(Wcg, WCGTh, WCGTl, 2048, 2048);
   k_split<<<32, 256, 0, stream>>>(query_v, QVh, QVl, 32768L);
   k_camb<<<dim3(8,32), 256, 0, stream>>>(cam_tab, cam_ids, CAMBh, CAMBl);
-  k_perm<<<1, 256, 0, stream>>>(subp, GIDX, SB);
-  k_wsoft<<<1, 64, 0, stream>>>(weights, WSM);
+  k_permw<<<1, 256, 0, stream>>>(subp, weights, GIDX, SB, WSM);
 
   gemm_nt_bsg<1,4,1,4><<<dim3(8,1,16), 256, 0, stream>>>(RQ0, QVh,QVl, WCQh,WCQl,
       16,2048,2048, 2048,2048,2048, 0,0,0, 1.f, nullptr,0, 16, PART);
@@ -912,40 +1083,32 @@
   k_softmax_plain_r<<<512, 256, 0, stream>>>(SREL, PART, 7, SCALE);
   k_pv2<<<dim3(4,32,7), 256, 16*44*4, stream>>>(F_REL, PART, SREL, 4608, 288, 44,
       GMIXh, GMIXl, 589824, nullptr);
-  k_reduce<<<1024, 256, 0, stream>>>(F_REL, PART, 1048576L, 6, 1.f);
-
-  k_rowstats<<<512, 256, 0, stream>>>(F_REL, 2048, 2048, MU_FR, M2_FR);
-  k_ln_apply_s<<<dim3(8,512), 256, 0, stream>>>(F_REL, MU_FR, M2_FR, QLNh, QLNl);
-  k_meanx<<<dim3(8,32), 256, 0, stream>>>(F_REL, MEANX);
-  k_rowstats<<<32,   256, 0, stream>>>(MEANX, 2048, 2048, MU_M, M2_M);
-  k_rowstats<<<2048, 256, 0, stream>>>(proto, 2048, 2048, MU_P, M2_P);
-  k_rowstats<<<2048, 256, 0, stream>>>(Wdg,   2048, 2048, MU_W, M2_W);
+  k_finalize_frel<<<512, 256, 0, stream>>>(F_REL, PART, 6, QLNh, QLNl);
+
+  k_meanx_stats<<<32, 256, 0, stream>>>(F_REL, MEANX, MU_M, M2_M);
+  k_rowstats2<<<4096, 256, 0, stream>>>(proto, Wdg, MU_P, M2_P, MU_W, M2_W);
   k_split<<<2048, 256, 0, stream>>>(Wdq, ROTh, ROTl, 4194304L);
   gemm_nt_bsg<2,2,2,2><<<dim3(32,8,3), 256, 0, stream>>>(RELQ2, QLNh,QLNl, ROTh,ROTl,
       512,2048,2048, 2048,2048,2048, 0,0,0, 1.f, nullptr,0, 3, PART);
   k_reduce_split<<<1024, 256, 0, stream>>>(RELQ2, PART, 1048576L, 2, 1.f, RELQ2h, RELQ2l);
   gemm_nt_mfma<1,4,1,4><<<dim3(8,2,8), 256, 0, stream>>>(PM, MEANX, proto, 32,2048,2048,
-      2048,2048,2048, 0,0,0, 1.f, nullptr,0, 8, PART, nullptr, nullptr);
-  k_reduce<<<256, 256, 0, stream>>>(PM, PART, 65536L, 7, 1.f);
-  k_sigma<<<dim3(8,32), 256, 0, stream>>>(PM, MU_P, M2_P, MU_M, M2_M, SIGMA);
+      2048,2048,2048, 0,0,0, 1.f, 8, PART);
+  k_sigma_r<<<dim3(8,32), 256, 0, stream>>>(PM, PART, 7, MU_P, M2_P, MU_M, M2_M, SIGMA);
   k_tr_split<<<dim3(64,64), dim3(32,8), 0, stream>>>(Wdg, ROTh, ROTl, 2048, 2048);
   gemm_nt_bsg<2,2,2,2><<<dim3(32,8,3), 256, 0, stream>>>(T1, RELQ2h,RELQ2l, ROTh,ROTl,
       512,2048,2048, 2048,2048,2048, 0,0,0, 1.f, nullptr,0, 3, PART);
   k_reduce_split<<<1024, 256, 0, stream>>>(T1, PART, 1048576L, 2, 1.f, T1h, T1l);
   gemm_nt_mfma<1,4,1,4><<<dim3(8,2,8), 256, 0, stream>>>(MX, MEANX, Wdg, 32,2048,2048,
-      2048,2048,2048, 0,0,0, 1.f, nullptr,0, 8, PART, nullptr, nullptr);
-  k_reduce<<<256, 256, 0, stream>>>(MX, PART, 65536L, 7, 1.f);
-  k_fixrow<<<dim3(8,32), 256, 0, stream>>>(MX, MU_M, MU_W);
+      2048,2048,2048, 0,0,0, 1.f, 8, PART_MX);
   k_split<<<2048, 256, 0, stream>>>(proto, ROTh, ROTl, 4194304L);
   gemm_nt_bsg<2,2,2,2><<<dim3(32,8,3), 256, 0, stream>>>(QP, T1h,T1l, ROTh,ROTl,
       512,2048,2048, 2048,2048,2048, 0,0,0, 1.f, nullptr,0, 3, PART);
-  k_reduce<<<1024, 256, 0, stream>>>(QP, PART, 1048576L, 2, 1.f);
-  k_qm2<<<512, 256, 0, stream>>>(RELQ2, MX, MU_W, QM, QW);
-  k_score2_s<<<512, 256, 0, stream>>>(QP, QM, QW, SIGMA, MU_P, QPWh, QPWl, W1, WMU, SCALE);
+  k_score2f<<<512, 256, 0, stream>>>(QP, PART, 2, RELQ2, MX, PART_MX, 7,
+      MU_W, MU_M, SIGMA, MU_P, QPWh, QPWl, W1, WMU, SCALE);
   k_tr_split<<<dim3(64,64), dim3(32,8), 0, stream>>>(proto, ROTh, ROTl, 2048, 2048);
   gemm_nt_bsg<2,2,2,2><<<dim3(32,8,3), 256, 0, stream>>>(OUT2, QPWh,QPWl, ROTh,ROTl,
       512,2048,2048, 2048,2048,2048, 0,0,0, 1.f, nullptr,0, 3, PART);
-  k_reduce<<<1024, 256, 0, stream>>>(OUT2, PART, 1048576L, 2, 1.f);
+  k_reduce4<<<1024, 256, 0, stream>>>(OUT2, PART, 1048576L, 2, 1.f);
   k_fpro_final_s<<<dim3(8,512), 256, 0, stream>>>(F_REL, OUT2, MEANX, MU_M, W1, WMU, WSM,
                                                   FPROh, FPROl, F_PRO);
 
@@ -960,7 +1123,7 @@
   k_softmax_plain_r<<<512, 256, 0, stream>>>(SREC, PART, 7, SCALE);
   k_pv2<<<dim3(4,32,7), 256, 16*44*4, stream>>>(F_REC, PART, SREC, 4608, 288, 44,
       GMIXh, GMIXl, 589824, nullptr);
-  k_reduce<<<1024, 256, 0, stream>>>(F_REC, PART, 1048576L, 6, 1.f);
+  k_reduce4<<<1024, 256, 0, stream>>>(F_REC, PART, 1048576L, 6, 1.f);
 
   gemm_nt_bsg<1,4,1,4><<<dim3(1,32,8), 256, 0, stream>>>(CC, RQW2h,RQW2l, CAMBh,CAMBl,
       512,32,2048, 2048,2048,32, 0,0,0, 1.f, nullptr,0, 8, PART_CC);
@@ -969,5 +1132,5 @@
   k_softmax_seg<<<512, 256, 0, stream>>>(SCOR, PART, 3, CC, PART_CC, 7, SB, SCALE);
   k_pv2<<<dim3(4,32,7), 256, 16*168*4, stream>>>(F_COR, PART, SCOR, 18432, 1152, 168,
       GMIXh, GMIXl, 589824, SB);
-  k_reduce<<<1024, 256, 0, stream>>>(F_COR, PART, 1048576L, 6, 1.f);
-}
+  k_reduce4<<<1024, 256, 0, stream>>>(F_COR, PART, 1048576L, 6, 1.f);
+}
```
